# Kernel optimization log

Measured on AMD Instinct MI355X. Metric: run time of the kernel, lower is better.

## Reference

```python
import jax, jax.numpy as jnp
import numpy as np

PSZ = 3      # patch_size
TOPK = 2     # topk candidates
EPS = 1e-12  # F.normalize eps


def extract_patches(x, psz, stride):
    """Torch unfold-style patch extraction: (B,C,H,W) -> (B, nH*nW, C, psz, psz)."""
    B, C, H, W = x.shape
    nH = (H - psz) // stride + 1
    nW = (W - psz) // stride + 1
    slices = []
    for di in range(psz):          # fixed 3x3 loop, not a data-dim loop
        for dj in range(psz):
            slices.append(x[:, :, di:di + (nH - 1) * stride + 1:stride,
                                  dj:dj + (nW - 1) * stride + 1:stride])
    p = jnp.stack(slices, axis=-1)                      # (B,C,nH,nW,psz*psz)
    p = p.reshape(B, C, nH, nW, psz, psz)
    p = p.transpose(0, 2, 3, 1, 4, 5).reshape(B, nH * nW, C, psz, psz)
    return p


def l2_normalize(x, axis):
    n = jnp.sqrt(jnp.sum(x * x, axis=axis, keepdims=True))
    return x / jnp.maximum(n, EPS)


def setup_inputs() -> dict:
    key = jax.random.key(0)
    k1, k2 = jax.random.split(key)
    pred_style = jax.random.normal(k1, (2, 128, 48, 48), dtype=jnp.float32)
    target_style = jax.random.normal(k2, (2 * TOPK, 128, 48, 48), dtype=jnp.float32)
    return {"pred_style": pred_style, "target_style": target_style}


def reference(pred_style, target_style):
    B = pred_style.shape[0]
    # raw patches (used for the final MSE / gather)
    tp = extract_patches(target_style, PSZ, 1)   # (B*TOPK, nT, C, 3, 3)
    pp = extract_patches(pred_style, PSZ, 1)     # (B, nQ, C, 3, 3)
    nT = tp.shape[1]

    # matching is done on channel-normalized features (F.normalize dim=1 / dim=2)
    p1n = extract_patches(l2_normalize(pred_style, axis=1), PSZ, 1)  # (B,nQ,C,3,3)
    tpn = l2_normalize(tp, axis=2).reshape(B, TOPK, nT, *tp.shape[2:])

    # cosine cross-correlation == conv with candidate patches as filters
    scores = jnp.einsum('bqcij,bkncij->bknq', p1n, tpn)  # (B,TOPK,nT,nQ)->(B,TOPK,nQ) reduce below

    sv = jnp.max(scores, axis=2)      # (B, TOPK, nQ) best value per candidate set
    si = jnp.argmax(scores, axis=2)   # (B, TOPK, nQ) best spatial idx per k
    k_idx = jnp.argmax(sv, axis=1)    # (B, nQ) best k per query position
    spatial = jnp.take_along_axis(si, k_idx[:, None, :], axis=1)[:, 0]  # (B, nQ)

    tpr = tp.reshape(B, TOPK, nT, *tp.shape[2:])
    bi = jnp.arange(B)[:, None]
    gathered = tpr[bi, k_idx, spatial]  # (B, nQ, C, 3, 3)

    return jnp.mean((pp - gathered) ** 2)
```

## Files before the change

### kernel.cpp

```cpp
#include <hip/hip_runtime.h>
#include <hip/hip_bf16.h>

typedef unsigned short u16;
typedef __attribute__((ext_vector_type(8))) short short8;
typedef __attribute__((ext_vector_type(4))) float f32x4;
typedef __attribute__((ext_vector_type(4))) unsigned int u32x4;

#define CC    128
#define WW    48
#define HW2   2304
#define NHW   46
#define NQ    2116
#define NPIX  2304
#define DSTRIDE ((size_t)NPIX * NPIX + 64)
#define BATCH 2
#define MT    126
#define NTC   190
#define DTS   200

__device__ __forceinline__ u16 f2bf(float f) {
  union { float f; unsigned u; } x; x.f = f;
  unsigned r = (x.u + 0x7fffu + ((x.u >> 16) & 1u)) >> 16;
  return (u16)r;
}
__device__ __forceinline__ float b2f(u16 v) {
  union { unsigned u; float f; } x; x.u = ((unsigned)v) << 16;
  return x.f;
}

__global__ __launch_bounds__(256) void k_norm(const float* __restrict__ pred,
                                              const float* __restrict__ targ,
                                              u16* __restrict__ PnT, u16* __restrict__ TnT) {
  const int img = blockIdx.y;
  const int p0  = blockIdx.x * 64;
  const int tid = threadIdx.x;
  const float* src = img < 2 ? pred + (size_t)img * CC * HW2
                             : targ + (size_t)(img - 2) * CC * HW2;
  u16* out = img < 2 ? PnT + (size_t)img * NPIX * CC
                     : TnT + (size_t)(img - 2) * NPIX * CC;

  __shared__ float sT[64][129];
  __shared__ float sInv[64];

  #pragma unroll
  for (int it = 0; it < 32; ++it) {
    int idx = it * 256 + tid;
    int c = idx >> 6, p = idx & 63;
    sT[p][c] = src[(size_t)c * HW2 + p0 + p];
  }
  __syncthreads();
  if (tid < 64) {
    float s = 0.f;
    for (int c = 0; c < CC; ++c) { float v = sT[tid][c]; s += v * v; }
    sInv[tid] = 1.0f / fmaxf(sqrtf(s), 1e-12f);
  }
  __syncthreads();
  #pragma unroll
  for (int it = 0; it < 4; ++it) {
    int cid = it * 256 + tid;
    int p = cid >> 4, g = cid & 15;
    int r = p0 + p;
    int sc = (g & ~7) | ((g & 7) ^ (r & 7));
    float inv = sInv[p];
    unsigned pack[4];
    #pragma unroll
    for (int e = 0; e < 8; ++e) {
      float v = sT[p][sc * 8 + e] * inv;
      if ((e & 1) == 0) pack[e >> 1] = (unsigned)f2bf(v);
      else              pack[e >> 1] |= ((unsigned)f2bf(v)) << 16;
    }
    u32x4 o; o.x = pack[0]; o.y = pack[1]; o.z = pack[2]; o.w = pack[3];
    *reinterpret_cast<u32x4*>(out + (size_t)r * CC + g * 8) = o;
  }
}

__global__ __launch_bounds__(512, 2) void k_pixdotH(const u16* __restrict__ PnT, const u16* __restrict__ TnT,
                                                    u16* __restrict__ H) {
  __shared__ u16 buf[40960];
  u16* sA = buf;
  u16* sB = buf + 16384;
  const int nt = blockIdx.x, mt = blockIdx.y, s = blockIdx.z;
  const int tid = threadIdx.x, lane = tid & 63, wid = tid >> 6;
  const int wm = wid >> 2, wn = wid & 3;
  const int r15 = lane & 15, g16 = lane >> 4;
  const int m0 = mt * MT, n0 = nt * NTC;

  const u16* Ab = PnT + (size_t)(s >> 1) * NPIX * CC;
  const u16* Bb = TnT + (size_t)s * NPIX * CC;
  u16* Hs = H + (size_t)s * DSTRIDE;

  #pragma unroll
  for (int i = 0; i < 4; ++i) {
    int sl = i * 512 + tid;
    int row = m0 + (sl >> 4); row = row < 2303 ? row : 2303;
    __builtin_amdgcn_global_load_lds(
      (const __attribute__((address_space(1))) unsigned*)(Ab + (size_t)row * CC + (sl & 15) * 8),
      (__attribute__((address_space(3))) unsigned*)&sA[sl * 8], 16, 0, 0);
  }
  #pragma unroll
  for (int i = 0; i < 6; ++i) {
    int sl = i * 512 + tid;
    int row = n0 + (sl >> 4); row = row < 2303 ? row : 2303;
    __builtin_amdgcn_global_load_lds(
      (const __attribute__((address_space(1))) unsigned*)(Bb + (size_t)row * CC + (sl & 15) * 8),
      (__attribute__((address_space(3))) unsigned*)&sB[sl * 8], 16, 0, 0);
  }

  f32x4 acc[4][3];
  const f32x4 z4 = {0.f, 0.f, 0.f, 0.f};
  #pragma unroll
  for (int i = 0; i < 4; ++i)
    #pragma unroll
    for (int j = 0; j < 3; ++j) acc[i][j] = z4;

  asm volatile("s_waitcnt vmcnt(0)" ::: "memory");
  __builtin_amdgcn_s_barrier();

  const int arow0 = wm * 64 + r15;
  const int brow0 = wn * 48 + r15;
  #pragma unroll
  for (int ks = 0; ks < 4; ++ks) {
    const int c = ks * 4 + g16;
    short8 af[4], bfv[3];
    #pragma unroll
    for (int mi = 0; mi < 4; ++mi) {
      int row = arow0 + mi * 16;
      int gr = m0 + row;
      af[mi] = *reinterpret_cast<const short8*>(
        &sA[row * 128 + (c >> 3) * 64 + (((c & 7) ^ (gr & 7)) * 8)]);
    }
    #pragma unroll
    for (int ni = 0; ni < 3; ++ni) {
      int row = brow0 + ni * 16;
      int gr = n0 + row;
      bfv[ni] = *reinterpret_cast<const short8*>(
        &sB[row * 128 + (c >> 3) * 64 + (((c & 7) ^ (gr & 7)) * 8)]);
    }
    __builtin_amdgcn_s_setprio(1);
    #pragma unroll
    for (int mi = 0; mi < 4; ++mi)
      #pragma unroll
      for (int ni = 0; ni < 3; ++ni)
        acc[mi][ni] = __builtin_amdgcn_mfma_f32_16x16x32_bf16(af[mi], bfv[ni], acc[mi][ni], 0, 0, 0);
    __builtin_amdgcn_s_setprio(0);
  }

  __syncthreads();
  u16* Dt = buf;
  #pragma unroll
  for (int mi = 0; mi < 4; ++mi)
    #pragma unroll
    for (int ni = 0; ni < 3; ++ni) {
      int col = wn * 48 + ni * 16 + r15;
      #pragma unroll
      for (int rg = 0; rg < 4; ++rg) {
        int row = wm * 64 + mi * 16 + g16 * 4 + rg;
        Dt[row * DTS + col] = f2bf(acc[mi][ni][rg]);
      }
    }
  __syncthreads();

  for (int t = tid; t < 126 * 24; t += 512) {
    int rr = t / 24, c8 = t - rr * 24;
    int grow = m0 + rr;
    if (grow >= 2302) continue;
    int lcol = c8 * 8;
    int lim = NTC - lcol;
    int glim = 2302 - (n0 + lcol);
    lim = lim < glim ? lim : glim;
    if (lim <= 0) continue;
    int base = rr * DTS + lcol;
    short8 a0 = *reinterpret_cast<const short8*>(&Dt[base]);
    short8 b0 = *reinterpret_cast<const short8*>(&Dt[base + DTS]);
    short8 b1 = *reinterpret_cast<const short8*>(&Dt[base + DTS + 8]);
    short8 c0 = *reinterpret_cast<const short8*>(&Dt[base + 2 * DTS]);
    short8 c1 = *reinterpret_cast<const short8*>(&Dt[base + 2 * DTS + 8]);
    short8 s1v = __builtin_shufflevector(b0, b1, 1, 2, 3, 4, 5, 6, 7, 8);
    short8 s2v = __builtin_shufflevector(c0, c1, 2, 3, 4, 5, 6, 7, 8, 9);
    unsigned pack[4];
    #pragma unroll
    for (int e = 0; e < 8; ++e) {
      float f = b2f((u16)a0[e]) + b2f((u16)s1v[e]) + b2f((u16)s2v[e]);
      if ((e & 1) == 0) pack[e >> 1] = (unsigned)f2bf(f);
      else              pack[e >> 1] |= ((unsigned)f2bf(f)) << 16;
    }
    u16* dst = Hs + (size_t)grow * NPIX + n0 + lcol;
    int nd = lim >= 8 ? 4 : (lim >> 1);
    #pragma unroll
    for (int d = 0; d < 4; ++d)
      if (d < nd) *reinterpret_cast<unsigned*>(dst + 2 * d) = pack[d];
  }
}

__global__ __launch_bounds__(512) void k_stencil(const u16* __restrict__ H,
                                                 const float* __restrict__ pred,
                                                 const float* __restrict__ targ,
                                                 float* __restrict__ msep) {
  const int bid = blockIdx.x;
  const int b = bid >= NQ ? 1 : 0;
  const int orig = bid - b * NQ;
  const int xcd = orig & 7, pos = orig >> 3;
  const int q = (xcd < 4 ? xcd * 265 : 1060 + (xcd - 4) * 264) + pos;

  const int tid = threadIdx.x, lane = tid & 63, wid = tid >> 6;
  const int qy = q / NHW, qx = q - qy * NHW;
  const int qp = qy * WW + qx;

  float best = -3.0e38f; int bidx = 0x7fffffff;
  #pragma unroll
  for (int it = 0; it < 2; ++it) {
    int t = it * 512 + tid;
    if (t < 552) {
      int kc = t / 276; int rem = t - kc * 276;
      int ny = rem / 6, cx = rem - ny * 6;
      const u16* Hs = H + (size_t)(b * 2 + kc) * DSTRIDE;
      int colb = ny * 48 + cx * 8;
      short8 t0 = *reinterpret_cast<const short8*>(Hs + (size_t)qp * NPIX + colb);
      short8 t1 = *reinterpret_cast<const short8*>(Hs + (size_t)(qp + 48) * NPIX + colb + 48);
      short8 t2 = *reinterpret_cast<const short8*>(Hs + (size_t)(qp + 96) * NPIX + colb + 96);
      int nbase = kc * NQ + ny * NHW + cx * 8;
      #pragma unroll
      for (int e = 0; e < 8; ++e) {
        float sc = b2f((u16)t0[e]) + b2f((u16)t1[e]) + b2f((u16)t2[e]);
        int n = nbase + e;
        bool take = (cx * 8 + e < NHW) &&
                    ((sc > best) || (sc == best && n < bidx));
        best = take ? sc : best;
        bidx = take ? n : bidx;
      }
    }
  }
  #pragma unroll
  for (int off = 1; off < 64; off <<= 1) {
    float ov = __shfl_xor(best, off, 64);
    int   oi = __shfl_xor(bidx, off, 64);
    bool take = (ov > best) || (ov == best && oi < bidx);
    best = take ? ov : best;
    bidx = take ? oi : bidx;
  }

  __shared__ float sv[8]; __shared__ int si[8];
  __shared__ float rsum[8];
  if (lane == 0) { sv[wid] = best; si[wid] = bidx; }
  __syncthreads();
  float fb = sv[0]; int fi = si[0];
  #pragma unroll
  for (int wv = 1; wv < 8; ++wv) {
    bool take = (sv[wv] > fb) || (sv[wv] == fb && si[wv] < fi);
    fb = take ? sv[wv] : fb;
    fi = take ? si[wv] : fi;
  }

  int nkc = fi >= NQ ? 1 : 0;
  int ns = fi - nkc * NQ;
  int ny = ns / NHW, nx = ns - ny * NHW;
  const float* P = pred + (size_t)b * CC * HW2;
  const float* T = targ + (size_t)(b * 2 + nkc) * CC * HW2;
  float ssum = 0.f;
  for (int i = tid; i < CC * 9; i += 512) {
    int c = i / 9, sp = i - 9 * c;
    int di = sp / 3, dj = sp - 3 * di;
    float d = P[(size_t)c * HW2 + (qy + di) * WW + qx + dj]
            - T[(size_t)c * HW2 + (ny + di) * WW + nx + dj];
    ssum += d * d;
  }
  #pragma unroll
  for (int off = 1; off < 64; off <<= 1) ssum += __shfl_xor(ssum, off, 64);
  if (lane == 0) rsum[wid] = ssum;
  __syncthreads();
  if (tid == 0) {
    float t = 0.f;
    #pragma unroll
    for (int wv = 0; wv < 8; ++wv) t += rsum[wv];
    msep[b * NQ + q] = t;
  }
}

__global__ void k_final(const float* __restrict__ msep, float* __restrict__ out) {
  int t = threadIdx.x;
  float s = 0.f;
  for (int i = t; i < BATCH * NQ; i += 256) s += msep[i];
  __shared__ float red[256];
  red[t] = s; __syncthreads();
  for (int st = 128; st > 0; st >>= 1) { if (t < st) red[t] += red[t + st]; __syncthreads(); }
  if (t == 0) out[0] = red[0] * (1.0f / 4875264.0f);
}

extern "C" void kernel_launch(void* const* d_in, const int* in_sizes, int n_in,
                              void* d_out, int out_size, void* d_ws, size_t ws_size,
                              hipStream_t stream) {
  const float* pred = (const float*)d_in[0];
  const float* targ = (const float*)d_in[1];
  char* ws = (char*)d_ws;

  size_t offP = 0;
  size_t offT = offP + (size_t)2 * NPIX * CC * 2;
  size_t offH = offT + (size_t)4 * NPIX * CC * 2;
  size_t offM = offH + (size_t)4 * DSTRIDE * 2;

  u16*   PnT  = (u16*)(ws + offP);
  u16*   TnT  = (u16*)(ws + offT);
  u16*   Hbuf = (u16*)(ws + offH);
  float* msep = (float*)(ws + offM);

  k_norm<<<dim3(36, 6), 256, 0, stream>>>(pred, targ, PnT, TnT);
  k_pixdotH<<<dim3(13, 19, 4), 512, 0, stream>>>(PnT, TnT, Hbuf);
  k_stencil<<<dim3(BATCH * NQ), 512, 0, stream>>>(Hbuf, pred, targ, msep);
  k_final<<<1, 256, 0, stream>>>(msep, (float*)d_out);
}
```

Measured before the change: 72.60 us.

## Store partial scores in fp16 and split argmax into packed max then index pass

Intermediate correlation sums are stored as fp16 instead of bf16, so the horizontal and vertical stencil adds become packed half-vector adds with no manual bf16 conversion. The argmax in the stencil kernel becomes two passes. The first is a packed fp16 max reduction over the block. The second reloads the scores, but only in waves that hold the maximum, and finds the smallest index that equals it. This removes per-element compare-and-select work on value/index pairs in exchange for a second global read in some waves. It also changes the numerics from bf16 to fp16 range and precision, which may alter tie-breaking or risk overflow.

```diff
diff --git a/kernel.cpp b/kernel.cpp
--- a/kernel.cpp
+++ b/kernel.cpp
@@ -3,6 +3,7 @@
 
 typedef unsigned short u16;
 typedef __attribute__((ext_vector_type(8))) short short8;
+typedef _Float16 half8 __attribute__((ext_vector_type(8)));
 typedef __attribute__((ext_vector_type(4))) float f32x4;
 typedef __attribute__((ext_vector_type(4))) unsigned int u32x4;
 
@@ -23,10 +24,6 @@
   unsigned r = (x.u + 0x7fffu + ((x.u >> 16) & 1u)) >> 16;
   return (u16)r;
 }
-__device__ __forceinline__ float b2f(u16 v) {
-  union { unsigned u; float f; } x; x.u = ((unsigned)v) << 16;
-  return x.f;
-}
 
 __global__ __launch_bounds__(256) void k_norm(const float* __restrict__ pred,
                                               const float* __restrict__ targ,
@@ -155,7 +152,7 @@
       #pragma unroll
       for (int rg = 0; rg < 4; ++rg) {
         int row = wm * 64 + mi * 16 + g16 * 4 + rg;
-        Dt[row * DTS + col] = f2bf(acc[mi][ni][rg]);
+        Dt[row * DTS + col] = __builtin_bit_cast(u16, (_Float16)acc[mi][ni][rg]);
       }
     }
   __syncthreads();
@@ -170,25 +167,20 @@
     lim = lim < glim ? lim : glim;
     if (lim <= 0) continue;
     int base = rr * DTS + lcol;
-    short8 a0 = *reinterpret_cast<const short8*>(&Dt[base]);
-    short8 b0 = *reinterpret_cast<const short8*>(&Dt[base + DTS]);
-    short8 b1 = *reinterpret_cast<const short8*>(&Dt[base + DTS + 8]);
-    short8 c0 = *reinterpret_cast<const short8*>(&Dt[base + 2 * DTS]);
-    short8 c1 = *reinterpret_cast<const short8*>(&Dt[base + 2 * DTS + 8]);
-    short8 s1v = __builtin_shufflevector(b0, b1, 1, 2, 3, 4, 5, 6, 7, 8);
-    short8 s2v = __builtin_shufflevector(c0, c1, 2, 3, 4, 5, 6, 7, 8, 9);
-    unsigned pack[4];
-    #pragma unroll
-    for (int e = 0; e < 8; ++e) {
-      float f = b2f((u16)a0[e]) + b2f((u16)s1v[e]) + b2f((u16)s2v[e]);
-      if ((e & 1) == 0) pack[e >> 1] = (unsigned)f2bf(f);
-      else              pack[e >> 1] |= ((unsigned)f2bf(f)) << 16;
-    }
+    half8 a0 = *reinterpret_cast<const half8*>(&Dt[base]);
+    half8 b0 = *reinterpret_cast<const half8*>(&Dt[base + DTS]);
+    half8 b1 = *reinterpret_cast<const half8*>(&Dt[base + DTS + 8]);
+    half8 c0 = *reinterpret_cast<const half8*>(&Dt[base + 2 * DTS]);
+    half8 c1 = *reinterpret_cast<const half8*>(&Dt[base + 2 * DTS + 8]);
+    half8 s1v = __builtin_shufflevector(b0, b1, 1, 2, 3, 4, 5, 6, 7, 8);
+    half8 s2v = __builtin_shufflevector(c0, c1, 2, 3, 4, 5, 6, 7, 8, 9);
+    half8 sum = a0 + s1v + s2v;
+    u32x4 pk = __builtin_bit_cast(u32x4, sum);
     u16* dst = Hs + (size_t)grow * NPIX + n0 + lcol;
     int nd = lim >= 8 ? 4 : (lim >> 1);
     #pragma unroll
     for (int d = 0; d < 4; ++d)
-      if (d < nd) *reinterpret_cast<unsigned*>(dst + 2 * d) = pack[d];
+      if (d < nd) *reinterpret_cast<unsigned*>(dst + 2 * d) = pk[d];
   }
 }
 
@@ -206,7 +198,9 @@
   const int qy = q / NHW, qx = q - qy * NHW;
   const int qp = qy * WW + qx;
 
-  float best = -3.0e38f; int bidx = 0x7fffffff;
+  const _Float16 ninf = __builtin_bit_cast(_Float16, (u16)0xFC00);
+  half8 pmax = {ninf, ninf, ninf, ninf, ninf, ninf, ninf, ninf};
+
   #pragma unroll
   for (int it = 0; it < 2; ++it) {
     int t = it * 512 + tid;
@@ -215,41 +209,66 @@
       int ny = rem / 6, cx = rem - ny * 6;
       const u16* Hs = H + (size_t)(b * 2 + kc) * DSTRIDE;
       int colb = ny * 48 + cx * 8;
-      short8 t0 = *reinterpret_cast<const short8*>(Hs + (size_t)qp * NPIX + colb);
-      short8 t1 = *reinterpret_cast<const short8*>(Hs + (size_t)(qp + 48) * NPIX + colb + 48);
-      short8 t2 = *reinterpret_cast<const short8*>(Hs + (size_t)(qp + 96) * NPIX + colb + 96);
-      int nbase = kc * NQ + ny * NHW + cx * 8;
-      #pragma unroll
-      for (int e = 0; e < 8; ++e) {
-        float sc = b2f((u16)t0[e]) + b2f((u16)t1[e]) + b2f((u16)t2[e]);
-        int n = nbase + e;
-        bool take = (cx * 8 + e < NHW) &&
-                    ((sc > best) || (sc == best && n < bidx));
-        best = take ? sc : best;
-        bidx = take ? n : bidx;
+      half8 t0 = *reinterpret_cast<const half8*>(Hs + (size_t)qp * NPIX + colb);
+      half8 t1 = *reinterpret_cast<const half8*>(Hs + (size_t)(qp + 48) * NPIX + colb + 48);
+      half8 t2 = *reinterpret_cast<const half8*>(Hs + (size_t)(qp + 96) * NPIX + colb + 96);
+      half8 sm = t0 + t1 + t2;
+      if (cx == 5) { sm[6] = ninf; sm[7] = ninf; }
+      pmax = __builtin_elementwise_max(pmax, sm);
+    }
+  }
+  float m = (float)pmax[0];
+  #pragma unroll
+  for (int e = 1; e < 8; ++e) { float v = (float)pmax[e]; m = v > m ? v : m; }
+  #pragma unroll
+  for (int off = 1; off < 64; off <<= 1) {
+    float o = __shfl_xor(m, off, 64);
+    m = o > m ? o : m;
+  }
+  __shared__ float sv[8];
+  __shared__ int si[8];
+  __shared__ float rsum[8];
+  if (lane == 0) sv[wid] = m;
+  __syncthreads();
+  float M = sv[0];
+  #pragma unroll
+  for (int wv = 1; wv < 8; ++wv) M = sv[wv] > M ? sv[wv] : M;
+
+  int nmin = 0x7fffffff;
+  if (m == M) {
+    #pragma unroll
+    for (int it = 0; it < 2; ++it) {
+      int t = it * 512 + tid;
+      if (t < 552) {
+        int kc = t / 276; int rem = t - kc * 276;
+        int ny = rem / 6, cx = rem - ny * 6;
+        const u16* Hs = H + (size_t)(b * 2 + kc) * DSTRIDE;
+        int colb = ny * 48 + cx * 8;
+        half8 t0 = *reinterpret_cast<const half8*>(Hs + (size_t)qp * NPIX + colb);
+        half8 t1 = *reinterpret_cast<const half8*>(Hs + (size_t)(qp + 48) * NPIX + colb + 48);
+        half8 t2 = *reinterpret_cast<const half8*>(Hs + (size_t)(qp + 96) * NPIX + colb + 96);
+        half8 sm = t0 + t1 + t2;
+        if (cx == 5) { sm[6] = ninf; sm[7] = ninf; }
+        int nbase = kc * NQ + ny * NHW + cx * 8;
+        #pragma unroll
+        for (int e = 0; e < 8; ++e) {
+          float sc = (float)sm[e];
+          int n = nbase + e;
+          if (sc == M && n < nmin) nmin = n;
+        }
       }
     }
   }
   #pragma unroll
   for (int off = 1; off < 64; off <<= 1) {
-    float ov = __shfl_xor(best, off, 64);
-    int   oi = __shfl_xor(bidx, off, 64);
-    bool take = (ov > best) || (ov == best && oi < bidx);
-    best = take ? ov : best;
-    bidx = take ? oi : bidx;
-  }
-
-  __shared__ float sv[8]; __shared__ int si[8];
-  __shared__ float rsum[8];
-  if (lane == 0) { sv[wid] = best; si[wid] = bidx; }
-  __syncthreads();
-  float fb = sv[0]; int fi = si[0];
-  #pragma unroll
-  for (int wv = 1; wv < 8; ++wv) {
-    bool take = (sv[wv] > fb) || (sv[wv] == fb && si[wv] < fi);
-    fb = take ? sv[wv] : fb;
-    fi = take ? si[wv] : fi;
-  }
+    int o = __shfl_xor(nmin, off, 64);
+    nmin = o < nmin ? o : nmin;
+  }
+  if (lane == 0) si[wid] = nmin;
+  __syncthreads();
+  int fi = si[0];
+  #pragma unroll
+  for (int wv = 1; wv < 8; ++wv) fi = si[wv] < fi ? si[wv] : fi;
 
   int nkc = fi >= NQ ? 1 : 0;
   int ns = fi - nkc * NQ;
```

Measured after the change: 70.24 us. -3.2%, faster.
